# Kernel optimization log

Measured on AMD Instinct MI355X. Metric: run time of the kernel, lower is better.

## Reference

```python
import jax, jax.numpy as jnp
import numpy as np

# config constants
B, T, C = 2, 2048, 1024
N_HEAD = 16
N_FULL = 8           # n_head - int(n_head * ratio_heads)
N_RED = 8            # int(n_head * 0.5)
HEAD_DIM = 64        # C // N_HEAD
RED_DIM = 32         # int(HEAD_DIM * 0.5)
WIN_FULL = 1024      # context_full
WIN_RED = 256        # context_reduced


def setup_inputs() -> dict:
    key = jax.random.key(0)
    ks = jax.random.split(key, 5)
    def w(k, shape, fan_in):
        return jax.random.normal(k, shape, jnp.float32) * (1.0 / np.sqrt(fan_in))
    return {
        "x": jax.random.normal(ks[0], (B, T, C), jnp.float32),
        "w_qkv_full": w(ks[1], (C, 3 * N_FULL * HEAD_DIM), C),
        "w_qk_red": w(ks[2], (C, 2 * N_RED * RED_DIM), C),
        "w_v_red": w(ks[3], (C, N_RED * HEAD_DIM), C),
        "w_proj": w(ks[4], (C, C), C),
    }


def _windowed_attn(q, k, v, window):
    # q,k: [B,H,T,dq], v: [B,H,T,dv]; causal sliding window: 0 <= i-j < window
    d = q.shape[-1]
    scores = jnp.einsum("bhqd,bhkd->bhqk", q, k) / jnp.sqrt(jnp.float32(d))
    i = jnp.arange(q.shape[2])[:, None]
    j = jnp.arange(k.shape[2])[None, :]
    mask = (i - j < 0) | (i - j >= window)
    scores = jnp.where(mask, -jnp.inf, scores)
    p = jax.nn.softmax(scores, axis=-1)
    return jnp.einsum("bhqk,bhkd->bhqd", p, v)


def reference(x, w_qkv_full, w_qk_red, w_v_red, w_proj):
    Bx, Tx, Cx = x.shape
    split_heads = lambda t, d: t.reshape(Bx, Tx, -1, d).transpose(0, 2, 1, 3)

    # full-dim heads
    q, k, v = jnp.split(x @ w_qkv_full, 3, axis=-1)
    y_full = _windowed_attn(split_heads(q, HEAD_DIM), split_heads(k, HEAD_DIM),
                            split_heads(v, HEAD_DIM), WIN_FULL)

    # reduced q/k dim heads (values keep full head_dim)
    qr, kr = jnp.split(x @ w_qk_red, 2, axis=-1)
    vr = x @ w_v_red
    y_red = _windowed_attn(split_heads(qr, RED_DIM), split_heads(kr, RED_DIM),
                           split_heads(vr, HEAD_DIM), WIN_RED)

    y = jnp.concatenate([y_full, y_red], axis=1)          # [B, n_head, T, head_dim]
    y = y.transpose(0, 2, 1, 3).reshape(Bx, Tx, Cx)
    return y @ w_proj
```

## Files before the change

### kernel.cpp

```cpp
#include <hip/hip_runtime.h>
#include <hip/hip_bf16.h>
#include <stdint.h>

#define TT 2048
#define BB 2
#define CC 1024
#define NEGF (-1e30f)

typedef short bf16x8 __attribute__((ext_vector_type(8)));
typedef short bf16x4 __attribute__((ext_vector_type(4)));
typedef float f32x4 __attribute__((ext_vector_type(4)));

__device__ __forceinline__ f32x4 mfma16(bf16x8 a, bf16x8 b, f32x4 c) {
  return __builtin_amdgcn_mfma_f32_16x16x32_bf16(a, b, c, 0, 0, 0);
}

__device__ __forceinline__ uint16_t f2bf(float f) {
  union { float f; uint32_t u; } v; v.f = f;
  uint32_t u = v.u;
  return (uint16_t)((u + 0x7FFFu + ((u >> 16) & 1u)) >> 16);
}

typedef __attribute__((address_space(3))) uint32_t lds_u32;
typedef const __attribute__((address_space(1))) uint32_t glb_u32;
__device__ __forceinline__ void gload_lds16(const uint16_t* g, uint16_t* l) {
  __builtin_amdgcn_global_load_lds((glb_u32*)g, (lds_u32*)l, 16, 0, 0);
}

__global__ __launch_bounds__(256) void k_convert(const float* __restrict__ in,
                                                 uint16_t* __restrict__ out, int n4) {
  int i = blockIdx.x * blockDim.x + threadIdx.x;
  if (i >= n4) return;
  float4 f = ((const float4*)in)[i];
  ushort4 o;
  o.x = f2bf(f.x); o.y = f2bf(f.y); o.z = f2bf(f.z); o.w = f2bf(f.w);
  ((ushort4*)out)[i] = o;
}

__global__ __launch_bounds__(256) void k_transpose(const float* __restrict__ W,
                                                   uint16_t* __restrict__ Wt,
                                                   int K, int N) {
  __shared__ float tile[32][33];
  int tx = threadIdx.x & 31, ty = threadIdx.x >> 5;
  int n0 = blockIdx.x * 32, k0 = blockIdx.y * 32;
#pragma unroll
  for (int r = 0; r < 4; r++)
    tile[ty + r * 8][tx] = W[(size_t)(k0 + ty + r * 8) * N + n0 + tx];
  __syncthreads();
#pragma unroll
  for (int r = 0; r < 4; r++)
    Wt[(size_t)(n0 + ty + r * 8) * K + k0 + tx] = f2bf(tile[tx][ty + r * 8]);
}

template <bool F32OUT>
__global__ __launch_bounds__(256) void k_gemm128(const uint16_t* __restrict__ A,
                                                 const uint16_t* __restrict__ Bt,
                                                 void* __restrict__ Cp,
                                                 int K, int ldc) {
  __shared__ __align__(16) uint16_t Alds[128 * 32];
  __shared__ __align__(16) uint16_t Blds[128 * 32];
  const int tid = threadIdx.x;
  const int lane = tid & 63, wave = tid >> 6;
  const int lr = lane & 15, lg = lane >> 4;
  const int wm = wave & 1, wn = wave >> 1;
  const int m0 = blockIdx.y * 128;
  const int n0 = blockIdx.x * 128;

  f32x4 acc[4][4] = {};

  const int srow = wave * 16 + (lane >> 2);
  const int scol = (lane & 3) * 8;
  const uint16_t* pa_l = A + (size_t)(m0 + srow) * K + scol;
  const uint16_t* pb_l = Bt + (size_t)(n0 + srow) * K + scol;
  uint16_t* alds_w0 = &Alds[(wave * 64) * 8];
  uint16_t* alds_w1 = &Alds[(256 + wave * 64) * 8];
  uint16_t* blds_w0 = &Blds[(wave * 64) * 8];
  uint16_t* blds_w1 = &Blds[(256 + wave * 64) * 8];

  for (int k0 = 0; k0 < K; k0 += 32) {
    __syncthreads();
    gload_lds16(pa_l + k0, alds_w0);
    gload_lds16(pa_l + (size_t)64 * K + k0, alds_w1);
    gload_lds16(pb_l + k0, blds_w0);
    gload_lds16(pb_l + (size_t)64 * K + k0, blds_w1);
    __syncthreads();

    bf16x8 af[4], bfr[4];
#pragma unroll
    for (int mi = 0; mi < 4; mi++)
      af[mi] = *(const bf16x8*)&Alds[(wm * 64 + mi * 16 + lr) * 32 + lg * 8];
#pragma unroll
    for (int ni = 0; ni < 4; ni++)
      bfr[ni] = *(const bf16x8*)&Blds[(wn * 64 + ni * 16 + lr) * 32 + lg * 8];
#pragma unroll
    for (int mi = 0; mi < 4; mi++)
#pragma unroll
      for (int ni = 0; ni < 4; ni++)
        acc[mi][ni] = mfma16(af[mi], bfr[ni], acc[mi][ni]);
  }

#pragma unroll
  for (int mi = 0; mi < 4; mi++)
#pragma unroll
    for (int ni = 0; ni < 4; ni++)
#pragma unroll
      for (int r = 0; r < 4; r++) {
        size_t idx = (size_t)(m0 + wm * 64 + mi * 16 + lg * 4 + r) * ldc
                   + n0 + wn * 64 + ni * 16 + lr;
        if (F32OUT) ((float*)Cp)[idx] = acc[mi][ni][r];
        else        ((uint16_t*)Cp)[idx] = f2bf(acc[mi][ni][r]);
      }
}

__global__ __launch_bounds__(256) void k_vtrans(const uint16_t* __restrict__ QKV,
                                                uint16_t* __restrict__ Vt) {
  __shared__ uint16_t tile[64][72];
  int t0 = blockIdx.x * 64;
  int h = blockIdx.y, b = blockIdx.z;
  int vOff = (h < 8) ? (1024 + h * 64) : (2048 + (h - 8) * 64);
  const uint16_t* src = QKV + ((size_t)b * TT + t0) * 2560 + vOff;
  int tx = threadIdx.x & 15, ty = threadIdx.x >> 4;
#pragma unroll
  for (int p = 0; p < 4; p++)
    *(ushort4*)&tile[ty + p * 16][tx * 4] =
        *(const ushort4*)(src + (size_t)(ty + p * 16) * 2560 + tx * 4);
  __syncthreads();
  uint16_t* dst = Vt + ((size_t)(b * 16 + h) * 64) * TT + t0;
#pragma unroll
  for (int p = 0; p < 4; p++) {
    int dv = ty + p * 16;
    ushort4 o;
    o.x = tile[tx * 4 + 0][dv];
    o.y = tile[tx * 4 + 1][dv];
    o.z = tile[tx * 4 + 2][dv];
    o.w = tile[tx * 4 + 3][dv];
    *(ushort4*)(dst + (size_t)dv * TT + tx * 4) = o;
  }
}

__global__ __launch_bounds__(256) void k_attn(const uint16_t* __restrict__ QKV,
                                              const uint16_t* __restrict__ Vt,
                                              uint16_t* __restrict__ Y) {
  __shared__ __align__(16) uint16_t Klds[2][64 * 64];
  __shared__ __align__(16) uint16_t Vlds[2][64 * 64];
  __shared__ __align__(16) uint16_t Plds[4][16][72];
  const int tid = threadIdx.x;
  const int lane = tid & 63, wave = tid >> 6;
  const int lr = lane & 15, lg = lane >> 4;
  const int qt = blockIdx.x & 31;
  const int h = (blockIdx.x >> 5) & 15;
  const int b = blockIdx.x >> 9;
  const int q0b = qt * 64;
  const int q0 = q0b + wave * 16;

  int dqk, window, qOff, kOff;
  if (h < 8) { dqk = 64; window = 1024; qOff = h * 64; kOff = 512 + h * 64; }
  else { int hr = h - 8; dqk = 32; window = 256; qOff = 1536 + hr * 32; kOff = 1792 + hr * 32; }
  const float scale = (dqk == 64) ? 0.125f : 0.17677669529663687f;
  const uint16_t* base = QKV + (size_t)b * TT * 2560;
  const uint16_t* vt = Vt + ((size_t)(b * 16 + h) * 64) * TT;
  const int nf = dqk >> 5;

  bf16x8 qf[2];
  for (int s = 0; s < nf; s++)
    qf[s] = *(const bf16x8*)(base + (size_t)(q0 + lr) * 2560 + qOff + s * 32 + lg * 8);

  float m = NEGF, lsum = 0.f;
  f32x4 o[4] = {};

  int klo_b = q0b - window + 1; if (klo_b < 0) klo_b = 0; klo_b &= ~63;
  const int klo_w = (q0 - window + 1 < 0) ? 0 : (q0 - window + 1);
  const int khi_w = q0 + 15;
  const int q = q0 + lr;
  const int kend = q0b + 63;

  auto stage = [&](int k0, int buf) {
    if (nf == 2) {
#pragma unroll
      for (int j = 0; j < 2; j++) {
        int c = j * 256 + tid;
        int row = c >> 3, cl = c & 7, sc = cl ^ (row & 7);
        gload_lds16(base + (size_t)(k0 + row) * 2560 + kOff + sc * 8,
                    &Klds[buf][(j * 256 + wave * 64) * 8]);
      }
    } else {
      int row = tid >> 2, cl = tid & 3, sc = cl ^ (row & 3);
      gload_lds16(base + (size_t)(k0 + row) * 2560 + kOff + sc * 8,
                  &Klds[buf][(wave * 64) * 8]);
    }
#pragma unroll
    for (int j = 0; j < 2; j++) {
      int c = j * 256 + tid;
      int row = c >> 3, cl = c & 7, sc = cl ^ (row & 7);
      gload_lds16(vt + (size_t)row * TT + k0 + sc * 8,
                  &Vlds[buf][(j * 256 + wave * 64) * 8]);
    }
  };

  stage(klo_b, 0);
  asm volatile("s_waitcnt vmcnt(0)" ::: "memory");
  __builtin_amdgcn_s_barrier();
  __builtin_amdgcn_sched_barrier(0);

  int cur = 0;
  for (int k0 = klo_b; k0 <= kend; k0 += 64) {
    const int nxt = k0 + 64;
    if (nxt <= kend) stage(nxt, cur ^ 1);

    if (!(k0 > khi_w || k0 + 63 < klo_w)) {
      f32x4 st[4];
      __builtin_amdgcn_s_setprio(1);
#pragma unroll
      for (int hh = 0; hh < 4; hh++) {
        f32x4 acc = {0.f, 0.f, 0.f, 0.f};
        int row = hh * 16 + lr;
        if (nf == 2) {
          acc = mfma16(*(const bf16x8*)&Klds[cur][row * 64 + ((lg) ^ (row & 7)) * 8], qf[0], acc);
          acc = mfma16(*(const bf16x8*)&Klds[cur][row * 64 + ((4 + lg) ^ (row & 7)) * 8], qf[1], acc);
        } else {
          acc = mfma16(*(const bf16x8*)&Klds[cur][row * 32 + ((lg) ^ (row & 3)) * 8], qf[0], acc);
        }
        st[hh] = acc;
      }
      __builtin_amdgcn_s_setprio(0);
      float tmax = NEGF;
      const bool interior = (k0 + 63 <= q0) && (q0 + 15 - k0 < window);
      if (interior) {
#pragma unroll
        for (int hh = 0; hh < 4; hh++)
#pragma unroll
          for (int r = 0; r < 4; r++) {
            float sv = st[hh][r] * scale;
            st[hh][r] = sv;
            tmax = fmaxf(tmax, sv);
          }
      } else {
#pragma unroll
        for (int hh = 0; hh < 4; hh++)
#pragma unroll
          for (int r = 0; r < 4; r++) {
            int key = k0 + 16 * hh + lg * 4 + r;
            bool ok = (key <= q) && (q - key < window);
            float sv = ok ? st[hh][r] * scale : NEGF;
            st[hh][r] = sv;
            tmax = fmaxf(tmax, sv);
          }
      }
      tmax = fmaxf(tmax, __shfl_xor(tmax, 16));
      tmax = fmaxf(tmax, __shfl_xor(tmax, 32));
      if (!__all(tmax <= m)) {
        float mn = fmaxf(m, tmax);
        float alpha = __expf(m - mn);
        lsum *= alpha;
#pragma unroll
        for (int d = 0; d < 4; d++) o[d] *= alpha;
        m = mn;
      }
      float psum = 0.f;
#pragma unroll
      for (int hh = 0; hh < 4; hh++) {
        bf16x4 pk;
#pragma unroll
        for (int r = 0; r < 4; r++) {
          float sv = st[hh][r];
          float p = (sv > -0.5e30f) ? __expf(sv - m) : 0.f;
          psum += p;
          pk[r] = (short)f2bf(p);
        }
        *(bf16x4*)&Plds[wave][lr][16 * hh + lg * 4] = pk;
      }
      psum += __shfl_xor(psum, 16);
      psum += __shfl_xor(psum, 32);
      lsum += psum;

      __builtin_amdgcn_s_setprio(1);
#pragma unroll
      for (int ks = 0; ks < 2; ks++) {
        bf16x8 pf = *(const bf16x8*)&Plds[wave][lr][ks * 32 + lg * 8];
#pragma unroll
        for (int db = 0; db < 4; db++) {
          int row = db * 16 + lr;
          bf16x8 vf = *(const bf16x8*)&Vlds[cur][row * 64 + ((4 * ks + lg) ^ (row & 7)) * 8];
          o[db] = mfma16(vf, pf, o[db]);
        }
      }
      __builtin_amdgcn_s_setprio(0);
    }

    asm volatile("s_waitcnt vmcnt(0)" ::: "memory");
    __builtin_amdgcn_sched_barrier(0);
    __builtin_amdgcn_s_barrier();
    __builtin_amdgcn_sched_barrier(0);
    cur ^= 1;
  }
  const float inv = 1.0f / lsum;
  uint16_t* yp = Y + ((size_t)b * TT + q0 + lr) * CC + h * 64;
#pragma unroll
  for (int db = 0; db < 4; db++)
#pragma unroll
    for (int r = 0; r < 4; r++)
      yp[db * 16 + lg * 4 + r] = f2bf(o[db][r] * inv);
}

extern "C" void kernel_launch(void* const* d_in, const int* in_sizes, int n_in,
                              void* d_out, int out_size, void* d_ws, size_t ws_size,
                              hipStream_t stream) {
  const float* x    = (const float*)d_in[0];
  const float* wqkv = (const float*)d_in[1];
  const float* wqk  = (const float*)d_in[2];
  const float* wv   = (const float*)d_in[3];
  const float* wp   = (const float*)d_in[4];

  uint16_t* ws  = (uint16_t*)d_ws;
  uint16_t* xb  = ws;
  uint16_t* WtA = xb  + (size_t)4096 * 1024;
  uint16_t* WtP = WtA + (size_t)2560 * 1024;
  uint16_t* QKV = WtP + (size_t)1024 * 1024;
  uint16_t* Yb  = QKV + (size_t)4096 * 2560;
  uint16_t* Vt  = xb;

  k_convert<<<4096, 256, 0, stream>>>(x, xb, 4096 * 1024 / 4);
  k_transpose<<<dim3(48, 32), 256, 0, stream>>>(wqkv, WtA, 1024, 1536);
  k_transpose<<<dim3(16, 32), 256, 0, stream>>>(wqk, WtA + (size_t)1536 * 1024, 1024, 512);
  k_transpose<<<dim3(16, 32), 256, 0, stream>>>(wv,  WtA + (size_t)2048 * 1024, 1024, 512);
  k_transpose<<<dim3(32, 32), 256, 0, stream>>>(wp,  WtP, 1024, 1024);
  k_gemm128<false><<<dim3(20, 32), 256, 0, stream>>>(xb, WtA, QKV, 1024, 2560);
  k_vtrans<<<dim3(32, 16, 2), 256, 0, stream>>>(QKV, Vt);
  k_attn<<<1024, 256, 0, stream>>>(QKV, Vt, Yb);
  k_gemm128<true><<<dim3(8, 32), 256, 0, stream>>>(Yb, WtP, (float*)d_out, 1024, 1024);
}
```

Baseline: 204.6 us.

## Double-buffer GEMM LDS, reverse attention block order, use exp2 softmax

The GEMM now double-buffers its A/B LDS tiles and prefetches the next K-slice before computing the current one, using one barrier per iteration instead of two. The attention kernel remaps block indices so the heaviest (late) query tiles launch first, with head types grouped. The softmax folds the scale into an exp2 argument through an FMA, drops the masked-score branch, splits the row sum across independent accumulators, and uses round-half-up bf16 conversion. These changes add LDS pressure in the GEMM and slightly alter rounding.

```diff
diff --git a/kernel.cpp b/kernel.cpp
--- a/kernel.cpp
+++ b/kernel.cpp
@@ -19,6 +19,10 @@
   union { float f; uint32_t u; } v; v.f = f;
   uint32_t u = v.u;
   return (uint16_t)((u + 0x7FFFu + ((u >> 16) & 1u)) >> 16);
+}
+__device__ __forceinline__ uint16_t f2bf_fast(float f) {
+  union { float f; uint32_t u; } v; v.f = f;
+  return (uint16_t)((v.u + 0x8000u) >> 16);
 }
 
 typedef __attribute__((address_space(3))) uint32_t lds_u32;
@@ -57,8 +61,8 @@
                                                  const uint16_t* __restrict__ Bt,
                                                  void* __restrict__ Cp,
                                                  int K, int ldc) {
-  __shared__ __align__(16) uint16_t Alds[128 * 32];
-  __shared__ __align__(16) uint16_t Blds[128 * 32];
+  __shared__ __align__(16) uint16_t Alds[2][128 * 32];
+  __shared__ __align__(16) uint16_t Blds[2][128 * 32];
   const int tid = threadIdx.x;
   const int lane = tid & 63, wave = tid >> 6;
   const int lr = lane & 15, lg = lane >> 4;
@@ -72,31 +76,41 @@
   const int scol = (lane & 3) * 8;
   const uint16_t* pa_l = A + (size_t)(m0 + srow) * K + scol;
   const uint16_t* pb_l = Bt + (size_t)(n0 + srow) * K + scol;
-  uint16_t* alds_w0 = &Alds[(wave * 64) * 8];
-  uint16_t* alds_w1 = &Alds[(256 + wave * 64) * 8];
-  uint16_t* blds_w0 = &Blds[(wave * 64) * 8];
-  uint16_t* blds_w1 = &Blds[(256 + wave * 64) * 8];
-
+
+  auto stage = [&](int k0, int buf) {
+    gload_lds16(pa_l + k0, &Alds[buf][(wave * 64) * 8]);
+    gload_lds16(pa_l + (size_t)64 * K + k0, &Alds[buf][(256 + wave * 64) * 8]);
+    gload_lds16(pb_l + k0, &Blds[buf][(wave * 64) * 8]);
+    gload_lds16(pb_l + (size_t)64 * K + k0, &Blds[buf][(256 + wave * 64) * 8]);
+  };
+
+  stage(0, 0);
+  asm volatile("s_waitcnt vmcnt(0)" ::: "memory");
+  __builtin_amdgcn_s_barrier();
+  __builtin_amdgcn_sched_barrier(0);
+
+  int cur = 0;
   for (int k0 = 0; k0 < K; k0 += 32) {
-    __syncthreads();
-    gload_lds16(pa_l + k0, alds_w0);
-    gload_lds16(pa_l + (size_t)64 * K + k0, alds_w1);
-    gload_lds16(pb_l + k0, blds_w0);
-    gload_lds16(pb_l + (size_t)64 * K + k0, blds_w1);
-    __syncthreads();
+    if (k0 + 32 < K) stage(k0 + 32, cur ^ 1);
 
     bf16x8 af[4], bfr[4];
 #pragma unroll
     for (int mi = 0; mi < 4; mi++)
-      af[mi] = *(const bf16x8*)&Alds[(wm * 64 + mi * 16 + lr) * 32 + lg * 8];
+      af[mi] = *(const bf16x8*)&Alds[cur][(wm * 64 + mi * 16 + lr) * 32 + lg * 8];
 #pragma unroll
     for (int ni = 0; ni < 4; ni++)
-      bfr[ni] = *(const bf16x8*)&Blds[(wn * 64 + ni * 16 + lr) * 32 + lg * 8];
+      bfr[ni] = *(const bf16x8*)&Blds[cur][(wn * 64 + ni * 16 + lr) * 32 + lg * 8];
 #pragma unroll
     for (int mi = 0; mi < 4; mi++)
 #pragma unroll
       for (int ni = 0; ni < 4; ni++)
         acc[mi][ni] = mfma16(af[mi], bfr[ni], acc[mi][ni]);
+
+    asm volatile("s_waitcnt vmcnt(0)" ::: "memory");
+    __builtin_amdgcn_sched_barrier(0);
+    __builtin_amdgcn_s_barrier();
+    __builtin_amdgcn_sched_barrier(0);
+    cur ^= 1;
   }
 
 #pragma unroll
@@ -147,9 +161,10 @@
   const int tid = threadIdx.x;
   const int lane = tid & 63, wave = tid >> 6;
   const int lr = lane & 15, lg = lane >> 4;
-  const int qt = blockIdx.x & 31;
-  const int h = (blockIdx.x >> 5) & 15;
-  const int b = blockIdx.x >> 9;
+
+  int idx = blockIdx.x, b, h, qt;
+  if (idx < 512) { qt = 31 - (idx >> 4); h = (idx >> 1) & 7; b = idx & 1; }
+  else { int j = idx - 512; qt = 31 - (j >> 4); h = 8 + ((j >> 1) & 7); b = j & 1; }
   const int q0b = qt * 64;
   const int q0 = q0b + wave * 16;
 
@@ -157,6 +172,7 @@
   if (h < 8) { dqk = 64; window = 1024; qOff = h * 64; kOff = 512 + h * 64; }
   else { int hr = h - 8; dqk = 32; window = 256; qOff = 1536 + hr * 32; kOff = 1792 + hr * 32; }
   const float scale = (dqk == 64) ? 0.125f : 0.17677669529663687f;
+  const float cl2 = scale * 1.44269504f;
   const uint16_t* base = QKV + (size_t)b * TT * 2560;
   const uint16_t* vt = Vt + ((size_t)(b * 16 + h) * 64) * TT;
   const int nf = dqk >> 5;
@@ -223,52 +239,48 @@
         st[hh] = acc;
       }
       __builtin_amdgcn_s_setprio(0);
-      float tmax = NEGF;
       const bool interior = (k0 + 63 <= q0) && (q0 + 15 - k0 < window);
-      if (interior) {
-#pragma unroll
-        for (int hh = 0; hh < 4; hh++)
-#pragma unroll
-          for (int r = 0; r < 4; r++) {
-            float sv = st[hh][r] * scale;
-            st[hh][r] = sv;
-            tmax = fmaxf(tmax, sv);
-          }
-      } else {
+      if (!interior) {
 #pragma unroll
         for (int hh = 0; hh < 4; hh++)
 #pragma unroll
           for (int r = 0; r < 4; r++) {
             int key = k0 + 16 * hh + lg * 4 + r;
             bool ok = (key <= q) && (q - key < window);
-            float sv = ok ? st[hh][r] * scale : NEGF;
-            st[hh][r] = sv;
-            tmax = fmaxf(tmax, sv);
+            st[hh][r] = ok ? st[hh][r] : NEGF;
           }
+      }
+      float tmax = NEGF;
+#pragma unroll
+      for (int hh = 0; hh < 4; hh++) {
+        float t01 = fmaxf(st[hh][0], st[hh][1]);
+        float t23 = fmaxf(st[hh][2], st[hh][3]);
+        tmax = fmaxf(tmax, fmaxf(t01, t23));
       }
       tmax = fmaxf(tmax, __shfl_xor(tmax, 16));
       tmax = fmaxf(tmax, __shfl_xor(tmax, 32));
       if (!__all(tmax <= m)) {
         float mn = fmaxf(m, tmax);
-        float alpha = __expf(m - mn);
+        float alpha = exp2f((m - mn) * cl2);
         lsum *= alpha;
 #pragma unroll
         for (int d = 0; d < 4; d++) o[d] *= alpha;
         m = mn;
       }
-      float psum = 0.f;
+      const float mc = fmaxf(m, -1e20f) * cl2;
+      f32x4 ps = {0.f, 0.f, 0.f, 0.f};
 #pragma unroll
       for (int hh = 0; hh < 4; hh++) {
         bf16x4 pk;
 #pragma unroll
         for (int r = 0; r < 4; r++) {
-          float sv = st[hh][r];
-          float p = (sv > -0.5e30f) ? __expf(sv - m) : 0.f;
-          psum += p;
-          pk[r] = (short)f2bf(p);
+          float p = exp2f(__builtin_fmaf(st[hh][r], cl2, -mc));
+          ps[r] += p;
+          pk[r] = (short)f2bf_fast(p);
         }
         *(bf16x4*)&Plds[wave][lr][16 * hh + lg * 4] = pk;
       }
+      float psum = (ps[0] + ps[1]) + (ps[2] + ps[3]);
       psum += __shfl_xor(psum, 16);
       psum += __shfl_xor(psum, 32);
       lsum += psum;
```

Result: faster. 189.3 us (-7.5%).
